# Performance work log

Hardware: AMD Instinct MI355X
Metric: run time of the kernel (lower is better)

Reference implementation:

```python
import jax, jax.numpy as jnp
import numpy as np

B, T, C, HS = 8, 4096, 1024, 128

def setup_inputs() -> dict:
    key = jax.random.key(0)
    kx, kq, kk, kv = jax.random.split(key, 4)
    x = jax.random.normal(kx, (B, T, C), dtype=jnp.float32)
    # Linear weights stored as [in, out] so projection is x @ W
    Wq = jax.random.normal(kq, (C, HS), dtype=jnp.float32) * (C ** -0.5)
    Wk = jax.random.normal(kk, (C, HS), dtype=jnp.float32) * (C ** -0.5)
    Wv = jax.random.normal(kv, (C, HS), dtype=jnp.float32) * (C ** -0.5)
    return {"x": x, "Wq": Wq, "Wk": Wk, "Wv": Wv}

def reference(x, Wq, Wk, Wv):
    # one head of causal self-attention (dropout=0.0 -> identity)
    q = x @ Wq  # [B,T,HS]
    k = x @ Wk
    v = x @ Wv
    scale = q.shape[-1] ** -0.5
    scores = jnp.einsum('bqd,bkd->bqk', q, k) * scale  # [B,T,T]
    t = q.shape[1]
    causal = jnp.tril(jnp.ones((t, t), dtype=bool))
    scores = jnp.where(causal, scores, jnp.finfo(scores.dtype).min)
    weights = jax.nn.softmax(scores, axis=-1)
    out = jnp.einsum('bqk,bkd->bqd', weights, v)  # [B,T,HS]
    return out
```

## Files before the change

### kernel.cpp

```cpp
#include <hip/hip_runtime.h>
#include <hip/hip_bf16.h>

#define TB 8
#define TT 4096
#define TC 1024
#define THS 128

typedef __bf16 bf16;
typedef __attribute__((ext_vector_type(8))) __bf16 bf16x8;
typedef __attribute__((ext_vector_type(2))) __bf16 bf16x2;
typedef __attribute__((ext_vector_type(4))) float f32x4;
typedef __attribute__((ext_vector_type(16))) float f32x16;

__device__ __forceinline__ unsigned pkbf(float a, float b) {
    bf16x2 t = { (bf16)a, (bf16)b };
    return __builtin_bit_cast(unsigned, t);
}

__device__ __forceinline__ void gload16(const void* g, void* l) {
    __builtin_amdgcn_global_load_lds(
        (const __attribute__((address_space(1))) void*)g,
        (__attribute__((address_space(3))) void*)l, 16, 0, 0);
}

__global__ __launch_bounds__(256) void wt_kernel(const float* __restrict__ Wq,
                                                 const float* __restrict__ Wk,
                                                 const float* __restrict__ Wv,
                                                 bf16* __restrict__ Wt) {
    __shared__ float tile[64][65];
    const int tid = threadIdx.x;
    const int idx = blockIdx.x;
    const int w = idx >> 5;
    const int kt = (idx & 31) >> 1, ntb = idx & 1;
    const int k0 = kt * 64, n0 = ntb * 64;
    const float* W = (w == 0) ? Wq : (w == 1) ? Wk : Wv;
    #pragma unroll
    for (int i = 0; i < 4; i++) {
        int r = (tid >> 4) + i * 16;
        int c4 = (tid & 15) * 4;
        float4 x4 = *reinterpret_cast<const float4*>(&W[(long)(k0 + r) * 128 + n0 + c4]);
        tile[r][c4 + 0] = x4.x; tile[r][c4 + 1] = x4.y;
        tile[r][c4 + 2] = x4.z; tile[r][c4 + 3] = x4.w;
    }
    __syncthreads();
    const int n = tid >> 2, kk = (tid & 3) * 16;
    bf16 o[16];
    #pragma unroll
    for (int j = 0; j < 16; j++) o[j] = (bf16)tile[kk + j][n];
    bf16* dst = &Wt[(long)((w << 7) + n0 + n) * 1024 + k0 + kk];
    *reinterpret_cast<bf16x8*>(dst)     = *reinterpret_cast<bf16x8*>(&o[0]);
    *reinterpret_cast<bf16x8*>(dst + 8) = *reinterpret_cast<bf16x8*>(&o[8]);
}

__global__ __launch_bounds__(512, 4) void qkv_kernel(const float* __restrict__ x,
                                                     const bf16* __restrict__ Wt,
                                                     bf16* __restrict__ Q,
                                                     bf16* __restrict__ K,
                                                     bf16* __restrict__ V) {
    __shared__ __align__(1024) char smem[81920];
    const int tid = threadIdx.x;
    const int wave = tid >> 6, lane = tid & 63;
    const int lr = lane & 15, g = lane >> 4;
    const int qs = wave >> 2, ns = wave & 3;
    const long row0 = (long)blockIdx.x * 64;

    int xOff[2], xL[2];
    #pragma unroll
    for (int i = 0; i < 2; i++) {
        int D = wave * 2048 + i * 1024 + lane * 16;
        int r = D >> 8, c = D & 255;
        xOff[i] = r * 4096 + (c ^ (((r & 7) << 4) ^ (((r >> 3) & 1) << 7)));
        xL[i] = wave * 2048 + i * 1024;
    }
    int wOff[6], wL[6];
    #pragma unroll
    for (int i = 0; i < 6; i++) {
        int D = wave * 6144 + i * 1024 + lane * 16;
        int n = D >> 7, c = D & 127;
        wOff[i] = n * 2048 + (c ^ ((n & 7) << 4));
        wL[i] = wave * 6144 + i * 1024;
    }
    const char* xb = (const char*)x + row0 * 4096;
    const char* wb = (const char*)Wt;

    f32x4 acc[2][6] = {};

    {
        #pragma unroll
        for (int i = 0; i < 2; i++) gload16(xb + xOff[i], smem + xL[i]);
        #pragma unroll
        for (int i = 0; i < 6; i++) gload16(wb + wOff[i], smem + 32768 + wL[i]);
        #pragma unroll
        for (int i = 0; i < 2; i++) gload16(xb + 256 + xOff[i], smem + 16384 + xL[i]);
    }

    #pragma unroll 1
    for (int s = 0; s < 16; s++) {
        if (s < 15) asm volatile("s_waitcnt vmcnt(2)" ::: "memory");
        else        asm volatile("s_waitcnt vmcnt(0)" ::: "memory");
        __builtin_amdgcn_s_barrier();

        const char* xp = smem + (s & 1) * 16384;
        const char* wp = smem + 32768;
        bf16x8 a[2][2];
        #pragma unroll
        for (int ar = 0; ar < 2; ar++) {
            const int r = qs * 32 + ar * 16 + lr;
            const int rs = ((r & 7) << 4) ^ (((r >> 3) & 1) << 7);
            #pragma unroll
            for (int ks = 0; ks < 2; ks++) {
                f32x4 lo  = *reinterpret_cast<const f32x4*>(xp + r * 256 + ((ks * 128 + g * 32) ^ rs));
                f32x4 hi4 = *reinterpret_cast<const f32x4*>(xp + r * 256 + ((ks * 128 + g * 32 + 16) ^ rs));
                uint4 u;
                u.x = pkbf(lo[0], lo[1]);  u.y = pkbf(lo[2], lo[3]);
                u.z = pkbf(hi4[0], hi4[1]); u.w = pkbf(hi4[2], hi4[3]);
                a[ar][ks] = __builtin_bit_cast(bf16x8, u);
            }
        }
        __builtin_amdgcn_s_setprio(1);
        #pragma unroll
        for (int nt = 0; nt < 6; nt++) {
            const int n = ns * 96 + nt * 16 + lr;
            const int nsw = (n & 7) << 4;
            #pragma unroll
            for (int ks = 0; ks < 2; ks++) {
                bf16x8 bfr = *reinterpret_cast<const bf16x8*>(wp + n * 128 + ((ks * 64 + g * 16) ^ nsw));
                #pragma unroll
                for (int ar = 0; ar < 2; ar++)
                    acc[ar][nt] = __builtin_amdgcn_mfma_f32_16x16x32_bf16(a[ar][ks], bfr, acc[ar][nt], 0, 0, 0);
            }
        }
        __builtin_amdgcn_s_setprio(0);
        __builtin_amdgcn_s_barrier();

        if (s + 1 < 16) {
            #pragma unroll
            for (int i = 0; i < 6; i++)
                gload16(wb + (s + 1) * 128 + wOff[i], smem + 32768 + wL[i]);
        }
        if (s + 2 < 16) {
            #pragma unroll
            for (int i = 0; i < 2; i++)
                gload16(xb + (s + 2) * 256 + xOff[i], smem + (s & 1) * 16384 + xL[i]);
        }
    }

    const float qscale = 0.08838834764831845f;
    bf16* outs[3] = {Q, K, V};
    #pragma unroll
    for (int nt = 0; nt < 6; nt++) {
        const int col = ns * 96 + nt * 16 + lr;
        const int w = col >> 7, d = col & 127;
        #pragma unroll
        for (int ar = 0; ar < 2; ar++)
            #pragma unroll
            for (int r = 0; r < 4; r++) {
                float val = acc[ar][nt][r];
                if (w == 0) val *= qscale;
                long row = row0 + qs * 32 + ar * 16 + g * 4 + r;
                outs[w][row * 128 + d] = (bf16)val;
            }
    }
}

__global__ __launch_bounds__(256) void vtrans_kernel(const bf16* __restrict__ V,
                                                     bf16* __restrict__ Vtt) {
    __shared__ __align__(16) bf16 tile[64][136];
    const int tid = threadIdx.x;
    const int b = blockIdx.y;
    const int tt = blockIdx.x;
    const long ibase = ((long)b * TT + tt * 64) * 128;
    #pragma unroll
    for (int i = 0; i < 4; i++) {
        int slot = tid + 256 * i;
        int r = slot >> 4, c8 = (slot & 15) * 8;
        *reinterpret_cast<bf16x8*>(&tile[r][c8]) =
            *reinterpret_cast<const bf16x8*>(&V[ibase + r * 128 + c8]);
    }
    __syncthreads();
    #pragma unroll
    for (int i = 0; i < 4; i++) {
        int slot = tid + 256 * i;
        int d = slot >> 3, t8 = (slot & 7) * 8;
        bf16x8 v;
        #pragma unroll
        for (int j = 0; j < 8; j++) v[j] = tile[t8 + j][d];
        *reinterpret_cast<bf16x8*>(&Vtt[(((long)b * 64 + tt) * 128 + d) * 64 + t8]) = v;
    }
}

__global__ __launch_bounds__(512, 2) void attn_kernel(const bf16* __restrict__ Q,
                                                      const bf16* __restrict__ K,
                                                      const bf16* __restrict__ Vtt,
                                                      float* __restrict__ out) {
    __shared__ __align__(1024) char smem[131072];
    __shared__ float mlb[6 * 64];
    const int tid = threadIdx.x;
    const int wave = tid >> 6, lane = tid & 63;
    const int c = lane & 31, hi = lane >> 5;
    const int qs = wave >> 2, kvq = wave & 3;
    const int kswz = ((c & 7) << 4) ^ (((c >> 3) & 1) << 7);
    const int vswz = (c & 7) << 4;
    const int v = blockIdx.x >> 3, b = blockIdx.x & 7;
    const long base = (long)b * TT * 128;
    const char* Kb = (const char*)(K + base);
    const char* Vb = (const char*)Vtt + (long)b * (64 * 16384);

    int kOff[4], vOff[4], lOff[4];
    #pragma unroll
    for (int i = 0; i < 4; i++) {
        int D = wave * 4096 + i * 1024 + lane * 16;
        kOff[i] = (D & ~255) | ((D & 255) ^ (((D >> 8) & 7) << 4) ^ (((D >> 11) & 1) << 7));
        vOff[i] = (D & ~127) | ((D & 127) ^ (((D >> 7) & 7) << 4));
        lOff[i] = wave * 4096 + i * 1024;
    }

    #pragma unroll 1
    for (int ph = 0; ph < 2; ph++) {
        const int qt = ph ? 63 - v : v;
        const int nIt = (qt + 2) >> 1;
        const int q0w = qt * 64 + qs * 32;
        const int qa = q0w + c;

        bf16x8 qf[8];
        #pragma unroll
        for (int dw = 0; dw < 8; dw++)
            qf[dw] = *reinterpret_cast<const bf16x8*>(&Q[base + (long)qa * 128 + dw * 16 + hi * 8]);

        f32x16 O[4] = {};
        float m = -__builtin_inff(), l = 0.f;

        {
            #pragma unroll
            for (int i = 0; i < 4; i++) {
                gload16(Kb + kOff[i], smem + lOff[i]);
                gload16(Vb + vOff[i], smem + 65536 + lOff[i]);
            }
            if (nIt > 1) {
                #pragma unroll
                for (int i = 0; i < 4; i++) {
                    gload16(Kb + 32768 + kOff[i], smem + 32768 + lOff[i]);
                    gload16(Vb + 32768 + vOff[i], smem + 98304 + lOff[i]);
                }
            }
        }

        #pragma unroll 1
        for (int it = 0; it < nIt; it++) {
            const int bi = it & 1;
            char* kBuf = smem + bi * 32768;
            char* vBuf = smem + 65536 + bi * 32768;
            if (it + 1 < nIt) asm volatile("s_waitcnt vmcnt(8)" ::: "memory");
            else              asm volatile("s_waitcnt vmcnt(0)" ::: "memory");
            __builtin_amdgcn_s_barrier();

            const int kv0 = it * 128 + kvq * 32;
            if (kv0 <= q0w) {
                const char* kb = kBuf + kvq * 8192;
                const char* vb = vBuf + (kvq >> 1) * 16384;
                const int vcol0 = (kvq & 1) * 64;
                f32x16 S = {};
                __builtin_amdgcn_s_setprio(1);
                #pragma unroll
                for (int dw = 0; dw < 8; dw++) {
                    bf16x8 kf = *reinterpret_cast<const bf16x8*>(
                        kb + c * 256 + ((dw * 32 + hi * 16) ^ kswz));
                    S = __builtin_amdgcn_mfma_f32_32x32x16_bf16(kf, qf[dw], S, 0, 0, 0);
                }
                __builtin_amdgcn_s_setprio(0);
                if (kv0 == q0w) {
                    #pragma unroll
                    for (int i = 0; i < 16; i++) {
                        int kvr = kv0 + (i & 3) + 8 * (i >> 2) + 4 * hi;
                        if (kvr > qa) S[i] = -__builtin_inff();
                    }
                }
                float t8[8];
                #pragma unroll
                for (int i = 0; i < 8; i++) t8[i] = fmaxf(S[i], S[i + 8]);
                float t4a = fmaxf(t8[0], t8[4]), t4b = fmaxf(t8[1], t8[5]);
                float t4c = fmaxf(t8[2], t8[6]), t4d = fmaxf(t8[3], t8[7]);
                float pm = fmaxf(fmaxf(t4a, t4b), fmaxf(t4c, t4d));
                pm = fmaxf(pm, __shfl_xor(pm, 32, 64));
                if (!__all(pm - m <= 8.0f)) {
                    float mn = fmaxf(m, pm);
                    float fr = __expf(m - mn);
                    #pragma unroll
                    for (int dt = 0; dt < 4; dt++) O[dt] = O[dt] * fr;
                    l *= fr;
                    m = mn;
                }
                #pragma unroll
                for (int i = 0; i < 16; i++) S[i] = __expf(S[i] - m);
                float s8[8];
                #pragma unroll
                for (int i = 0; i < 8; i++) s8[i] = S[i] + S[i + 8];
                l += ((s8[0] + s8[4]) + (s8[1] + s8[5])) + ((s8[2] + s8[6]) + (s8[3] + s8[7]));

                bf16x8 pf[2];
                #pragma unroll
                for (int wl = 0; wl < 2; wl++) {
                    const int i0 = 8 * wl;
                    unsigned L0 = pkbf(S[i0 + 0], S[i0 + 1]);
                    unsigned L1 = pkbf(S[i0 + 2], S[i0 + 3]);
                    unsigned H0 = pkbf(S[i0 + 4], S[i0 + 5]);
                    unsigned H1 = pkbf(S[i0 + 6], S[i0 + 7]);
                    unsigned sel0 = hi ? L0 : H0;
                    unsigned sel1 = hi ? L1 : H1;
                    unsigned x0 = __shfl_xor((int)sel0, 32, 64);
                    unsigned x1 = __shfl_xor((int)sel1, 32, 64);
                    uint4 f;
                    f.x = hi ? x0 : L0;
                    f.y = hi ? x1 : L1;
                    f.z = hi ? H0 : x0;
                    f.w = hi ? H1 : x1;
                    pf[wl] = __builtin_bit_cast(bf16x8, f);
                }
                __builtin_amdgcn_s_setprio(1);
                #pragma unroll
                for (int wl = 0; wl < 2; wl++)
                    #pragma unroll
                    for (int dt = 0; dt < 4; dt++) {
                        bf16x8 vf = *reinterpret_cast<const bf16x8*>(
                            vb + (dt * 32 + c) * 128 + ((vcol0 + wl * 32 + hi * 16) ^ vswz));
                        O[dt] = __builtin_amdgcn_mfma_f32_32x32x16_bf16(vf, pf[wl], O[dt], 0, 0, 0);
                    }
                __builtin_amdgcn_s_setprio(0);
            }
            __builtin_amdgcn_s_barrier();
            if (it + 2 < nIt) {
                const char* Ks = Kb + (long)(it + 2) * 32768;
                const char* Vs = Vb + (long)(it + 2) * 32768;
                #pragma unroll
                for (int i = 0; i < 4; i++) {
                    gload16(Ks + kOff[i], kBuf + lOff[i]);
                    gload16(Vs + vOff[i], vBuf + lOff[i]);
                }
            }
        }

        l += __shfl_xor(l, 32, 64);

        if (kvq != 0) {
            const int sl = qs * 3 + (kvq - 1);
            char* om = smem + sl * 16384;
            #pragma unroll
            for (int dt = 0; dt < 4; dt++)
                #pragma unroll
                for (int g = 0; g < 4; g++) {
                    float4 w4 = { O[dt][4 * g + 0], O[dt][4 * g + 1],
                                  O[dt][4 * g + 2], O[dt][4 * g + 3] };
                    *reinterpret_cast<float4*>(
                        om + c * 512 + ((dt * 128 + g * 32 + hi * 16) ^ ((c & 7) << 4))) = w4;
                }
            if (hi == 0) { mlb[sl * 64 + c] = m; mlb[sl * 64 + 32 + c] = l; }
        }
        __syncthreads();
        if (kvq == 0) {
            float mq[3], lq[3];
            float mx = m;
            #pragma unroll
            for (int p = 0; p < 3; p++) {
                const int sl = qs * 3 + p;
                mq[p] = mlb[sl * 64 + c];
                lq[p] = mlb[sl * 64 + 32 + c];
                mx = fmaxf(mx, mq[p]);
            }
            float f0 = __expf(m - mx);
            float lt = l * f0;
            float fq[3];
            #pragma unroll
            for (int p = 0; p < 3; p++) { fq[p] = __expf(mq[p] - mx); lt += lq[p] * fq[p]; }
            float linv = 1.0f / lt;
            #pragma unroll
            for (int dt = 0; dt < 4; dt++)
                #pragma unroll
                for (int g = 0; g < 4; g++) {
                    float4 r;
                    r.x = O[dt][4 * g + 0] * f0;
                    r.y = O[dt][4 * g + 1] * f0;
                    r.z = O[dt][4 * g + 2] * f0;
                    r.w = O[dt][4 * g + 3] * f0;
                    #pragma unroll
                    for (int p = 0; p < 3; p++) {
                        const char* om = smem + (qs * 3 + p) * 16384;
                        float4 o1 = *reinterpret_cast<const float4*>(
                            om + c * 512 + ((dt * 128 + g * 32 + hi * 16) ^ ((c & 7) << 4)));
                        r.x += o1.x * fq[p]; r.y += o1.y * fq[p];
                        r.z += o1.z * fq[p]; r.w += o1.w * fq[p];
                    }
                    r.x *= linv; r.y *= linv; r.z *= linv; r.w *= linv;
                    *reinterpret_cast<float4*>(
                        &out[base + (long)qa * 128 + dt * 32 + 8 * g + 4 * hi]) = r;
                }
        }
        __syncthreads();
    }
}

extern "C" void kernel_launch(void* const* d_in, const int* in_sizes, int n_in,
                              void* d_out, int out_size, void* d_ws, size_t ws_size,
                              hipStream_t stream) {
    const float* x  = (const float*)d_in[0];
    const float* Wq = (const float*)d_in[1];
    const float* Wk = (const float*)d_in[2];
    const float* Wv = (const float*)d_in[3];
    float* out = (float*)d_out;
    bf16* Q   = (bf16*)d_ws;
    bf16* K   = Q   + (size_t)32768 * 128;
    bf16* V   = K   + (size_t)32768 * 128;
    bf16* Wt  = V   + (size_t)32768 * 128;
    bf16* Vtt = Wt  + (size_t)3 * 128 * 1024;
    wt_kernel<<<96, 256, 0, stream>>>(Wq, Wk, Wv, Wt);
    qkv_kernel<<<512, 512, 0, stream>>>(x, Wt, Q, K, V);
    vtrans_kernel<<<dim3(64, 8), 256, 0, stream>>>(V, Vtt);
    attn_kernel<<<256, 512, 0, stream>>>(Q, K, Vtt, out);
}
```

Before: 116.3 us.

## Fuse V transpose into QKV epilogue and stage outputs through LDS

The QKV projection epilogue now stages each of the Q, K and V output tiles through shared memory. Q and K are written with coalesced 16-byte stores, and V is written directly in the transposed tile layout the attention kernel consumes. This removes the separate vtrans kernel launch and the round trip of V through global memory. The cost is extra barriers and LDS traffic in the epilogue, plus a possible bank conflict on the transposed read.

```diff
diff --git a/kernel.cpp b/kernel.cpp
--- a/kernel.cpp
+++ b/kernel.cpp
@@ -56,7 +56,7 @@
                                                      const bf16* __restrict__ Wt,
                                                      bf16* __restrict__ Q,
                                                      bf16* __restrict__ K,
-                                                     bf16* __restrict__ V) {
+                                                     bf16* __restrict__ Vtt) {
     __shared__ __align__(1024) char smem[81920];
     const int tid = threadIdx.x;
     const int wave = tid >> 6, lane = tid & 63;
@@ -146,46 +146,47 @@
     }
 
     const float qscale = 0.08838834764831845f;
-    bf16* outs[3] = {Q, K, V};
-    #pragma unroll
-    for (int nt = 0; nt < 6; nt++) {
-        const int col = ns * 96 + nt * 16 + lr;
-        const int w = col >> 7, d = col & 127;
-        #pragma unroll
-        for (int ar = 0; ar < 2; ar++)
-            #pragma unroll
-            for (int r = 0; r < 4; r++) {
-                float val = acc[ar][nt][r];
-                if (w == 0) val *= qscale;
-                long row = row0 + qs * 32 + ar * 16 + g * 4 + r;
-                outs[w][row * 128 + d] = (bf16)val;
-            }
-    }
-}
-
-__global__ __launch_bounds__(256) void vtrans_kernel(const bf16* __restrict__ V,
-                                                     bf16* __restrict__ Vtt) {
-    __shared__ __align__(16) bf16 tile[64][136];
-    const int tid = threadIdx.x;
-    const int b = blockIdx.y;
-    const int tt = blockIdx.x;
-    const long ibase = ((long)b * TT + tt * 64) * 128;
-    #pragma unroll
-    for (int i = 0; i < 4; i++) {
-        int slot = tid + 256 * i;
-        int r = slot >> 4, c8 = (slot & 15) * 8;
-        *reinterpret_cast<bf16x8*>(&tile[r][c8]) =
-            *reinterpret_cast<const bf16x8*>(&V[ibase + r * 128 + c8]);
-    }
-    __syncthreads();
-    #pragma unroll
-    for (int i = 0; i < 4; i++) {
-        int slot = tid + 256 * i;
-        int d = slot >> 3, t8 = (slot & 7) * 8;
-        bf16x8 v;
-        #pragma unroll
-        for (int j = 0; j < 8; j++) v[j] = tile[t8 + j][d];
-        *reinterpret_cast<bf16x8*>(&Vtt[(((long)b * 64 + tt) * 128 + d) * 64 + t8]) = v;
+    bf16* ld = (bf16*)smem;
+    #pragma unroll 1
+    for (int wsel = 0; wsel < 3; wsel++) {
+        __syncthreads();
+        #pragma unroll
+        for (int nt = 0; nt < 6; nt++) {
+            const int colbase = ns * 96 + nt * 16;
+            if ((colbase >> 7) != wsel) continue;
+            const int d = (colbase + lr) & 127;
+            #pragma unroll
+            for (int ar = 0; ar < 2; ar++)
+                #pragma unroll
+                for (int r = 0; r < 4; r++) {
+                    float val = acc[ar][nt][r];
+                    if (wsel == 0) val *= qscale;
+                    const int lrow = qs * 32 + ar * 16 + g * 4 + r;
+                    ld[lrow * 136 + d] = (bf16)val;
+                }
+        }
+        __syncthreads();
+        if (wsel < 2) {
+            bf16* dst = (wsel == 0 ? Q : K) + row0 * 128;
+            #pragma unroll
+            for (int i = 0; i < 2; i++) {
+                const int slot = tid + 512 * i;
+                const int rr = slot >> 4, c8 = (slot & 15) * 8;
+                bf16x8 vv = *reinterpret_cast<const bf16x8*>(&ld[rr * 136 + c8]);
+                *reinterpret_cast<bf16x8*>(&dst[rr * 128 + c8]) = vv;
+            }
+        } else {
+            bf16* dst = Vtt + (long)blockIdx.x * 8192;
+            #pragma unroll
+            for (int i = 0; i < 2; i++) {
+                const int slot = tid + 512 * i;
+                const int d = slot >> 3, t8 = (slot & 7) * 8;
+                bf16x8 vv;
+                #pragma unroll
+                for (int j = 0; j < 8; j++) vv[j] = ld[(t8 + j) * 136 + d];
+                *reinterpret_cast<bf16x8*>(&dst[d * 64 + t8]) = vv;
+            }
+        }
     }
 }
 
@@ -408,11 +409,9 @@
     float* out = (float*)d_out;
     bf16* Q   = (bf16*)d_ws;
     bf16* K   = Q   + (size_t)32768 * 128;
-    bf16* V   = K   + (size_t)32768 * 128;
-    bf16* Wt  = V   + (size_t)32768 * 128;
-    bf16* Vtt = Wt  + (size_t)3 * 128 * 1024;
+    bf16* Vtt = K   + (size_t)32768 * 128;
+    bf16* Wt  = Vtt + (size_t)8 * 64 * 128 * 64;
     wt_kernel<<<96, 256, 0, stream>>>(Wq, Wk, Wv, Wt);
-    qkv_kernel<<<512, 512, 0, stream>>>(x, Wt, Q, K, V);
-    vtrans_kernel<<<dim3(64, 8), 256, 0, stream>>>(V, Vtt);
+    qkv_kernel<<<512, 512, 0, stream>>>(x, Wt, Q, K, Vtt);
     attn_kernel<<<256, 512, 0, stream>>>(Q, K, Vtt, out);
 }
```

Measured after the change: 114.1 us, median of 2. Within noise of the previous version (-1.9%).
